# Kernel tuning notes

Measured on AMD Instinct MI355X. Metric: run time of the kernel, lower is better.

## Reference

```python
import jax, jax.numpy as jnp
import numpy as np

N = 100_000      # atoms (nodes)
E = 1_600_000    # directed edges
F_IN = 89        # atom feature dim
H = 128          # hidden dim
P = 20_000       # polyhedra (N/P = 5 atoms each)
C = 500          # crystals (P/C = 40 polyhedra each)
OUT = 1
EPS = 1e-5


def setup_inputs() -> dict:
    key = jax.random.key(0)
    ks = jax.random.split(key, 10)
    x = jax.random.normal(ks[0], (N, F_IN), jnp.float32)
    edge_index = jax.random.randint(ks[1], (2, E), 0, N)
    # sorted segment ids guaranteeing non-empty segments (faithful to PyG Batch layout)
    batch = jnp.repeat(jnp.arange(P), N // P)          # node -> polyhedron
    crystal_ids = jnp.repeat(jnp.arange(C), P // C)    # polyhedron -> crystal
    # GCNConv weights (glorot-ish) and biases; conv0 maps 89->128, convs 1..4 map 128->128
    W0 = jax.random.normal(ks[2], (F_IN, H), jnp.float32) * (1.0 / np.sqrt(F_IN))
    Ws = jax.random.normal(ks[3], (4, H, H), jnp.float32) * (1.0 / np.sqrt(H))
    bs = jnp.zeros((5, H), jnp.float32)
    # 5 BatchNorm layers
    gammas = jnp.ones((5, H), jnp.float32)
    betas = jnp.zeros((5, H), jnp.float32)
    # predictor MLP
    Wp1 = jax.random.normal(ks[4], (H, H), jnp.float32) * (1.0 / np.sqrt(H))
    bp1 = jnp.zeros((H,), jnp.float32)
    Wp2 = jax.random.normal(ks[5], (H, OUT), jnp.float32) * (1.0 / np.sqrt(H))
    bp2 = jnp.zeros((OUT,), jnp.float32)
    return dict(x=x, edge_index=edge_index, batch=batch, crystal_ids=crystal_ids,
                W0=W0, Ws=Ws, bs=bs, gammas=gammas, betas=betas,
                Wp1=Wp1, bp1=bp1, Wp2=Wp2, bp2=bp2)


def _bn(h, g, b):
    # BatchNorm1d, training mode: biased batch statistics over nodes
    mu = jnp.mean(h, axis=0)
    var = jnp.var(h, axis=0)
    return g * (h - mu) * jax.lax.rsqrt(var + EPS) + b


def reference(x, edge_index, batch, crystal_ids, W0, Ws, bs, gammas, betas, Wp1, bp1, Wp2, bp2):
    # --- GCN normalization with self-loops (shared by all 5 convs) ---
    loops = jnp.arange(N)
    src = jnp.concatenate([edge_index[0], loops])   # [E+N]
    dst = jnp.concatenate([edge_index[1], loops])
    deg = jax.ops.segment_sum(jnp.ones_like(src, jnp.float32), dst, num_segments=N)
    dinv = jnp.where(deg > 0, jax.lax.rsqrt(deg), 0.0)
    norm = (dinv[src] * dinv[dst])[:, None]          # [E+N, 1]

    def conv(h, W, b):
        m = h @ W                                    # [N, H]
        agg = jax.ops.segment_sum(m[src] * norm, dst, num_segments=N)
        return agg + b

    h = jax.nn.relu(_bn(conv(x, W0, bs[0]), gammas[0], betas[0]))
    for i in range(4):
        h = jax.nn.relu(_bn(conv(h, Ws[i], bs[i + 1]), gammas[i + 1], betas[i + 1]))

    # global_mean_pool over polyhedra
    cnt_p = jax.ops.segment_sum(jnp.ones((N,), jnp.float32), batch, num_segments=P)
    poly = jax.ops.segment_sum(h, batch, num_segments=P) / cnt_p[:, None]

    # per-crystal mean of polyhedron reps (vectorized form of the Python loop)
    cnt_c = jax.ops.segment_sum(jnp.ones((P,), jnp.float32), crystal_ids, num_segments=C)
    crys = jax.ops.segment_sum(poly, crystal_ids, num_segments=C) / cnt_c[:, None]

    # predictor MLP (Dropout is identity at inference)
    pred = jax.nn.relu(crys @ Wp1 + bp1) @ Wp2 + bp2   # [C, 1]
    return pred
```

## Files before the change

### kernel.cpp

```cpp
#include <hip/hip_runtime.h>

#define N_ATOMS 100000
#define N_EDGES 1600000
#define F_INDIM 89
#define N_CRYS  500
#define EPSBN   1e-5f
#define DRANGE  12500
#define RBLK    250
#define NSB     400
#define CAPSEG  28160
#define GRP     128
#define NGRP    782
#define B1E     2048
#define NBIN    104
#define IMGMAX  12288

typedef unsigned short u16;
typedef unsigned int   u32;
typedef unsigned long long u64;
typedef __attribute__((ext_vector_type(8))) short short8;
typedef __attribute__((ext_vector_type(4))) float f32x4;
typedef __attribute__((ext_vector_type(4))) unsigned int u32x4;

__device__ __forceinline__ float bf2f(u16 u){ union{u32 i; float f;} v; v.i=((u32)u)<<16; return v.f; }
__device__ __forceinline__ float bflo(u32 u){ union{u32 i; float f;} v; v.i=u<<16; return v.f; }
__device__ __forceinline__ float bfhi(u32 u){ union{u32 i; float f;} v; v.i=u&0xffff0000u; return v.f; }
__device__ __forceinline__ u16 f2bf(float f){
  u32 x=__float_as_uint(f);
  return (u16)((x + 0x7fffu + ((x>>16)&1u))>>16);
}
__device__ __forceinline__ u32 pack2(float a, float b){ return (u32)f2bf(a) | ((u32)f2bf(b)<<16); }
__device__ __forceinline__ float ldf(const void* p, int i, int m){
  return m ? ((const float*)p)[i] : bf2f(((const u16*)p)[i]);
}
__device__ __forceinline__ int fpmode(const void* gammas){ return (((const u16*)gammas)[0]==0) ? 1 : 0; }

__global__ __launch_bounds__(256) void k_bucket(const int* __restrict__ ei, u64* __restrict__ bkt,
                                                int* __restrict__ bcnt, int* __restrict__ degi8){
  __shared__ int lcnt[8], loff[8], lbase[8];
  __shared__ u64 lval[256];
  __shared__ int ldst[256];
  int t = threadIdx.x;
  int seg = blockIdx.x & 7;
  int e = blockIdx.x*256 + t;
  if (t < 8) lcnt[t] = 0;
  __syncthreads();
  int d=0, s=0, rr=0, li=0;
  bool valid = (e < N_EDGES);
  if (valid){
    d = ei[N_EDGES+e]; if ((u32)d >= N_ATOMS) d = 0;
    s = ei[e];         if ((u32)s >= N_ATOMS) s = 0;
    rr = d / DRANGE;
    li = atomicAdd(&lcnt[rr], 1);
    atomicAdd(&degi8[seg*N_ATOMS + d], 1);
  }
  __syncthreads();
  if (t == 0){ int run=0; for (int b=0;b<8;b++){ loff[b]=run; run+=lcnt[b]; } }
  __syncthreads();
  if (t < 8 && lcnt[t] > 0)
    lbase[t] = atomicAdd(&bcnt[seg*64 + t], lcnt[t]);
  __syncthreads();
  if (valid){
    int p = loff[rr] + li;
    lval[p] = ((u64)(u32)d << 32) | (u32)s;
    ldst[p] = (seg*8 + rr)*CAPSEG + lbase[rr] + li;
  }
  __syncthreads();
  int tot = loff[7] + lcnt[7];
  if (t < tot) bkt[ldst[t]] = lval[t];
}

__global__ void k_hist(const int* __restrict__ degi8, int* __restrict__ degi,
                       int* __restrict__ hist, int* __restrict__ blockHist){
  __shared__ int lh[256];
  int t = threadIdx.x, b = blockIdx.x;
  lh[t] = 0; __syncthreads();
  if (t < RBLK){
    int n = b*RBLK + t;
    int dg = 0;
    #pragma unroll
    for (int k=0;k<8;k++) dg += degi8[k*N_ATOMS + n];
    degi[n] = dg;
    atomicAdd(&lh[dg>255?255:dg], 1);
  }
  __syncthreads();
  blockHist[b*256 + t] = lh[t];
  if (lh[t]) atomicAdd(&hist[(b/50)*256 + t], lh[t]);
}

__global__ void k_hist_scan(int* __restrict__ hist){
  __shared__ int s[256];
  int R = blockIdx.x, t = threadIdx.x;
  int own = hist[R*256+t]; s[t] = own; __syncthreads();
  for (int k=1;k<256;k<<=1){ int a=(t>=k)?s[t-k]:0; __syncthreads(); s[t]+=a; __syncthreads(); }
  hist[R*256+t] = s[t] - own;
}

__global__ __launch_bounds__(64) void k_blockoff(const int* __restrict__ blockHist, const int* __restrict__ binBase,
                                                 int* __restrict__ blockOff){
  int bid = blockIdx.x;
  int c = bid & 255, R = bid >> 8;
  int t = threadIdx.x;
  int own = (t<50) ? blockHist[(R*50+t)*256 + c] : 0;
  int v = own;
  #pragma unroll
  for (int k=1;k<64;k<<=1){ int u = __shfl_up(v, k, 64); if (t>=k) v += u; }
  if (t<50) blockOff[(R*50+t)*256 + c] = R*DRANGE + binBase[R*256 + c] + (v - own);
}

__global__ void k_rank(const int* __restrict__ degi, const int* __restrict__ blockOff,
                       int* __restrict__ nodeAt, int* __restrict__ rankOf,
                       float* __restrict__ dinv, float* __restrict__ dinvR){
  __shared__ int boff[256];
  __shared__ int cnt[256];
  int b = blockIdx.x, t = threadIdx.x;
  boff[t] = blockOff[b*256 + t];
  cnt[t] = 0;
  __syncthreads();
  if (t >= RBLK) return;
  int n = b*RBLK + t;
  int dg = degi[n];
  int cd = dg>255?255:dg;
  int li = atomicAdd(&cnt[cd], 1);
  int r = boff[cd] + li;
  nodeAt[r] = n; rankOf[n] = r;
  float di = rsqrtf((float)(dg + 1));
  dinv[n] = di; dinvR[r] = di;
}

__global__ __launch_bounds__(256) void k_scan_partial(const int* __restrict__ degi, const int* __restrict__ nodeAt,
                                                      int* __restrict__ bsum){
  int b=blockIdx.x, t=threadIdx.x;
  int s=0;
  #pragma unroll
  for (int j=0;j<4;j++){
    int i=b*1024 + j*256 + t;
    if(i<N_ATOMS){
      int dg = degi[nodeAt[i]];
      s += (dg+3)&~3;
    }
  }
  __shared__ int red[256];
  red[t]=s; __syncthreads();
  for (int k=128;k>0;k>>=1){ if(t<k) red[t]+=red[t+k]; __syncthreads(); }
  if (t==0) bsum[b]=red[0];
}

__global__ void k_scan_bsum(int* __restrict__ bsum, int nb){
  __shared__ int s[128];
  int t=threadIdx.x;
  int own = (t<nb)? bsum[t]:0;
  s[t]=own; __syncthreads();
  for (int k=1;k<128;k<<=1){ int a=(t>=k)?s[t-k]:0; __syncthreads(); s[t]+=a; __syncthreads(); }
  if (t<nb) bsum[t]=s[t]-own;
}

__global__ __launch_bounds__(256) void k_scan_write(const int* __restrict__ degi, const int* __restrict__ nodeAt,
                                                    const int* __restrict__ bsum,
                                                    int* __restrict__ off){
  int b=blockIdx.x, t=threadIdx.x;
  int base=b*1024+t*4;
  int v[4], s=0;
  #pragma unroll
  for (int j=0;j<4;j++){ int i=base+j; v[j]=(i<N_ATOMS)?((degi[nodeAt[i]]+3)&~3):0; s+=v[j]; }
  __shared__ int ts[256];
  ts[t]=s; __syncthreads();
  for (int k=1;k<256;k<<=1){ int a=(t>=k)?ts[t-k]:0; __syncthreads(); ts[t]+=a; __syncthreads(); }
  int run = ts[t]-s + bsum[b];
  #pragma unroll
  for (int j=0;j<4;j++){
    int i=base+j;
    if (i<=N_ATOMS) off[i]=run;
    run+=v[j];
  }
}

__global__ __launch_bounds__(256) void k_group(const u64* __restrict__ bkt, const int* __restrict__ bcnt,
                                               const int* __restrict__ rankOf, const int* __restrict__ off,
                                               int* __restrict__ cnt2, u64* __restrict__ bkt2){
  __shared__ int lcnt[NBIN], loff[NBIN], gb[NBIN];
  __shared__ u64 lval[B1E];
  __shared__ int ldst[B1E];
  const int t = threadIdx.x;
  const int rr = blockIdx.x & 7;
  const int rest = blockIdx.x >> 3;
  const int seg = rest & 7, ch = rest >> 3;
  const int cnt = bcnt[seg*64 + rr];
  const int e0 = ch*B1E;
  int nloc = cnt - e0; if (nloc < 0) nloc = 0; if (nloc > B1E) nloc = B1E;
  const int g0 = (rr*DRANGE) >> 7;
  if (t < NBIN){ lcnt[t] = 0; }
  __syncthreads();
  const u64* src = bkt + (size_t)(seg*8 + rr)*CAPSEG + e0;
  int rk8[8], s8[8], sl8[8];
  #pragma unroll
  for (int j=0;j<8;j++){
    int i = j*256 + t;
    rk8[j] = -1;
    if (i < nloc){
      u64 v = src[i];
      int rk = rankOf[(int)(v>>32)];
      rk8[j] = rk; s8[j] = (int)(u32)v;
      sl8[j] = atomicAdd(&lcnt[(rk>>7) - g0], 1);
    }
  }
  __syncthreads();
  if (t == 0){
    int run = 0;
    for (int b=0;b<NBIN;b++){ loff[b] = run; run += lcnt[b]; }
  }
  __syncthreads();
  if (t < NBIN && lcnt[t] > 0){
    int g = g0 + t;
    gb[t] = off[g*GRP] + atomicAdd(&cnt2[g], lcnt[t]);
  }
  __syncthreads();
  #pragma unroll
  for (int j=0;j<8;j++){
    if (rk8[j] >= 0){
      int rel = (rk8[j]>>7) - g0;
      int p = loff[rel] + sl8[j];
      lval[p] = ((u64)(u32)rk8[j] << 32) | (u32)s8[j];
      ldst[p] = gb[rel] + sl8[j];
    }
  }
  __syncthreads();
  for (int i=t; i<nloc; i+=256)
    bkt2[ldst[i]] = lval[i];
}

__global__ __launch_bounds__(256) void k_csr(const u64* __restrict__ bkt2, const int* __restrict__ cnt2,
                                             const int* __restrict__ off, u32* __restrict__ csrS){
  __shared__ u32 img[IMGMAX];
  __shared__ int lcur[GRP];
  const int g = blockIdx.x, t = threadIdx.x;
  const int r0 = g*GRP;
  const int r1 = (r0+GRP < N_ATOMS) ? r0+GRP : N_ATOMS;
  const int base = off[r0];
  const int size = off[r1] - base;
  const int n = cnt2[g];
  if (size <= IMGMAX){
    for (int i=t; i<size; i+=256) img[i] = (u32)N_ATOMS;
    if (t < r1-r0) lcur[t] = off[r0+t] - base;
    __syncthreads();
    for (int i=t; i<n; i+=256){
      u64 v = bkt2[(size_t)base + i];
      int p = atomicAdd(&lcur[(int)(v>>32) - r0], 1);
      img[p] = (u32)v;
    }
    __syncthreads();
    uint4* c4 = (uint4*)(csrS + base);
    const uint4* i4 = (const uint4*)img;
    for (int i=t; i<(size>>2); i+=256) c4[i] = i4[i];
  } else {
    if (t < r1-r0) lcur[t] = off[r0+t];
    for (int i=t; i<size; i+=256) csrS[base+i] = (u32)N_ATOMS;
    __syncthreads();
    for (int i=t; i<n; i+=256){
      u64 v = bkt2[(size_t)base + i];
      int p = atomicAdd(&lcur[(int)(v>>32) - r0], 1);
      csrS[p] = (u32)v;
    }
  }
}

__global__ void k_packW(const void* __restrict__ W0, const void* __restrict__ Ws,
                        const void* __restrict__ gammas, u16* __restrict__ dst){
  int L    = blockIdx.x >> 3;
  int tid  = (blockIdx.x & 7)*256 + threadIdx.x;
  int K    = (L==0) ? F_INDIM : 128;
  int Kpad = (L==0) ? 96 : 128;
  if (tid >= (Kpad/32)*8*64) return;
  const void* W = (L==0) ? W0 : Ws;
  int woff = (L==0) ? 0 : (L-1)*128*128;
  int fp32m = fpmode(gammas);
  int lane = tid & 63, sc = tid >> 6;
  int c = sc & 7, s = sc >> 3;
  u16 vals[8];
  #pragma unroll
  for (int j=0;j<8;j++){
    int k  = s*32 + (lane>>4)*8 + j;
    int ch = c*16 + (lane&15);
    float v = (k<K) ? ldf(W, woff + k*128 + ch, fp32m) : 0.f;
    vals[j] = f2bf(v);
  }
  u16* out = dst + (size_t)L*16384;
  *(ushort4*)&out[tid*8]   = *(const ushort4*)&vals[0];
  *(ushort4*)&out[tid*8+4] = *(const ushort4*)&vals[4];
}

#define AROW 136
__global__ __launch_bounds__(256) void k_gemm_mfma(const u16* __restrict__ inA, const void* __restrict__ inX,
                                                   int K, int Kpad, const u16* __restrict__ Wpk,
                                                   const float* __restrict__ statsPrev, int useAct,
                                                   const float* __restrict__ dinv,
                                                   u16* __restrict__ mout,
                                                   const void* __restrict__ gammas,
                                                   const void* __restrict__ betas, int goff){
  __shared__ __align__(16) u16 Al[128*AROW];
  __shared__ float cl[256];
  const int t = threadIdx.x, lane = t & 63, w = t >> 6;
  const int tile = blockIdx.x * 128;

  if (useAct){
    if (t < 128){
      int fp32m = fpmode(gammas);
      float mu  = statsPrev[t] * (1.f/N_ATOMS);
      float var = statsPrev[128+t] * (1.f/N_ATOMS) - mu*mu;
      if (var < 0.f) var = 0.f;
      float sc = ldf(gammas, goff+t, fp32m) / sqrtf(var + EPSBN);
      cl[t]     = sc;
      cl[128+t] = ldf(betas, goff+t, fp32m) - sc*mu;
    }
    __syncthreads();
    const uint4* HA4 = (const uint4*)inA;
    for (int idx=t; idx<128*16; idx+=256){
      int node = idx>>4, q = idx&15;
      int gn = tile+node;
      uint4 v = (gn<N_ATOMS) ? HA4[((size_t)(q>>2)*(N_ATOMS+1) + gn)*4 + (q&3)] : make_uint4(0,0,0,0);
      int kk = q*8;
      u16 r[8];
      r[0]=f2bf(fmaxf(fmaf(cl[kk+0], bflo(v.x), cl[128+kk+0]),0.f));
      r[1]=f2bf(fmaxf(fmaf(cl[kk+1], bfhi(v.x), cl[128+kk+1]),0.f));
      r[2]=f2bf(fmaxf(fmaf(cl[kk+2], bflo(v.y), cl[128+kk+2]),0.f));
      r[3]=f2bf(fmaxf(fmaf(cl[kk+3], bfhi(v.y), cl[128+kk+3]),0.f));
      r[4]=f2bf(fmaxf(fmaf(cl[kk+4], bflo(v.z), cl[128+kk+4]),0.f));
      r[5]=f2bf(fmaxf(fmaf(cl[kk+5], bfhi(v.z), cl[128+kk+5]),0.f));
      r[6]=f2bf(fmaxf(fmaf(cl[kk+6], bflo(v.w), cl[128+kk+6]),0.f));
      r[7]=f2bf(fmaxf(fmaf(cl[kk+7], bfhi(v.w), cl[128+kk+7]),0.f));
      *(uint4*)&Al[node*AROW + kk] = *(const uint4*)&r[0];
    }
  } else {
    int fp32m = fpmode(gammas);
    for (int idx=t; idx<128*96; idx+=256){
      int node = idx/96, kk = idx - node*96;
      int gn = tile+node;
      float v = (kk<K && gn<N_ATOMS) ? ldf(inX, gn*K+kk, fp32m) : 0.f;
      Al[node*AROW + kk] = f2bf(v);
    }
  }
  __syncthreads();

  f32x4 acc[2][8];
  #pragma unroll
  for (int rr=0;rr<2;rr++)
    #pragma unroll
    for (int c=0;c<8;c++) acc[rr][c] = (f32x4){0.f,0.f,0.f,0.f};
  const int row = lane & 15, quad = lane >> 4;

  const int nstep = Kpad >> 5;
  for (int s=0; s<nstep; ++s){
    short8 a0 = *(const short8*)&Al[(w*32+row)*AROW    + s*32 + quad*8];
    short8 a1 = *(const short8*)&Al[(w*32+16+row)*AROW + s*32 + quad*8];
    #pragma unroll
    for (int c=0;c<8;c++){
      short8 b = *(const short8*)&Wpk[(size_t)((s*8+c)*64 + lane)*8];
      acc[0][c] = __builtin_amdgcn_mfma_f32_16x16x32_bf16(a0, b, acc[0][c], 0, 0, 0);
      acc[1][c] = __builtin_amdgcn_mfma_f32_16x16x32_bf16(a1, b, acc[1][c], 0, 0, 0);
    }
  }
  __syncthreads();
  float di[2][4];
  #pragma unroll
  for (int rr=0;rr<2;rr++)
    #pragma unroll
    for (int r=0;r<4;r++){
      int gn = tile + w*32 + rr*16 + quad*4 + r;
      di[rr][r] = (gn<N_ATOMS) ? dinv[gn] : 0.f;
    }
  #pragma unroll
  for (int rr=0;rr<2;rr++)
    #pragma unroll
    for (int c=0;c<8;c++)
      #pragma unroll
      for (int r=0;r<4;r++){
        int node = w*32 + rr*16 + quad*4 + r, ch = c*16 + row;
        Al[node*AROW + ch] = f2bf(di[rr][r]*acc[rr][c][r]);
      }
  __syncthreads();
  for (int idx=t; idx<2048; idx+=256){
    int blk = idx>>9, rem = idx&511, node = rem>>2, part = rem&3;
    int gn = tile+node;
    if (gn < N_ATOMS){
      uint4 v = *(const uint4*)&Al[node*AROW + blk*32 + part*8];
      *(uint4*)&mout[((size_t)blk*(N_ATOMS+1) + gn)*32 + part*8] = v;
    }
  }
  if (blockIdx.x == gridDim.x-1 && t < 16){
    int blk = t>>2, part = t&3;
    *(uint4*)&mout[((size_t)blk*(N_ATOMS+1) + N_ATOMS)*32 + part*8] = make_uint4(0,0,0,0);
  }
}

#define ACC8(r) do{ a[0]+=bflo(r.x); a[1]+=bfhi(r.x); a[2]+=bflo(r.y); a[3]+=bfhi(r.y); \
                    a[4]+=bflo(r.z); a[5]+=bfhi(r.z); a[6]+=bflo(r.w); a[7]+=bfhi(r.w);}while(0)
__global__ __launch_bounds__(256) void k_agg(const u16* __restrict__ m_, const u32* __restrict__ csrS,
                                             const int* __restrict__ off, const int* __restrict__ nodeAt,
                                             const float* __restrict__ dinvR,
                                             u16* __restrict__ agg_, float* __restrict__ stats){
  const int t = threadIdx.x, lane = t & 63, w = t >> 6;
  const int par = lane & 3, p = lane >> 2;
  const int cls = blockIdx.x & 7;
  const int slice = cls >> 1, half = cls & 1;
  const int r = half*50000 + (int)(blockIdx.x >> 3)*64 + w*16 + p;
  const int rlim = half*50000 + 50000;

  const uint4* m4   = (const uint4*)m_ + (size_t)slice*(N_ATOMS+1)*4;
  uint4*       agg4 = (uint4*)agg_     + (size_t)slice*(N_ATOMS+1)*4;

  float a[8], q8[8];
  #pragma unroll
  for (int i=0;i<8;i++){ a[i]=0.f; q8[i]=0.f; }

  if (r < rlim){
    int n = nodeAt[r];
    uint4 sv = m4[(size_t)n*4 + par];
    ACC8(sv);
    int e   = off[r];
    int end = off[r+1];
    if ((end - e) & 4){
      u32x4 iv = *(const u32x4*)(csrS+e);
      uint4 g0 = m4[(size_t)iv[0]*4 + par];
      uint4 g1 = m4[(size_t)iv[1]*4 + par];
      uint4 g2 = m4[(size_t)iv[2]*4 + par];
      uint4 g3 = m4[(size_t)iv[3]*4 + par];
      ACC8(g0); ACC8(g1); ACC8(g2); ACC8(g3);
      e += 4;
    }
    if (e < end){
      u32x4 i0 = *(const u32x4*)(csrS+e), i1 = *(const u32x4*)(csrS+e+4);
      uint4 A0 = m4[(size_t)i0[0]*4 + par];
      uint4 A1 = m4[(size_t)i0[1]*4 + par];
      uint4 A2 = m4[(size_t)i0[2]*4 + par];
      uint4 A3 = m4[(size_t)i0[3]*4 + par];
      uint4 A4 = m4[(size_t)i1[0]*4 + par];
      uint4 A5 = m4[(size_t)i1[1]*4 + par];
      uint4 A6 = m4[(size_t)i1[2]*4 + par];
      uint4 A7 = m4[(size_t)i1[3]*4 + par];
      e += 8;
      bool more = (e < end);
      while (true){
        uint4 B0,B1,B2,B3,B4,B5,B6,B7;
        if (more){
          u32x4 j0 = *(const u32x4*)(csrS+e), j1 = *(const u32x4*)(csrS+e+4);
          B0 = m4[(size_t)j0[0]*4 + par];
          B1 = m4[(size_t)j0[1]*4 + par];
          B2 = m4[(size_t)j0[2]*4 + par];
          B3 = m4[(size_t)j0[3]*4 + par];
          B4 = m4[(size_t)j1[0]*4 + par];
          B5 = m4[(size_t)j1[1]*4 + par];
          B6 = m4[(size_t)j1[2]*4 + par];
          B7 = m4[(size_t)j1[3]*4 + par];
          e += 8;
        }
        ACC8(A0); ACC8(A1); ACC8(A2); ACC8(A3);
        ACC8(A4); ACC8(A5); ACC8(A6); ACC8(A7);
        if (!more) break;
        A0=B0; A1=B1; A2=B2; A3=B3; A4=B4; A5=B5; A6=B6; A7=B7;
        more = (e < end);
      }
    }
    float di = dinvR[r];
    #pragma unroll
    for (int i=0;i<8;i++){ a[i]*=di; q8[i]=a[i]*a[i]; }
    u32x4 o;
    o[0] = pack2(a[0],a[1]); o[1] = pack2(a[2],a[3]);
    o[2] = pack2(a[4],a[5]); o[3] = pack2(a[6],a[7]);
    __builtin_nontemporal_store(o, (u32x4*)&agg4[(size_t)n*4 + par]);
  }
  #pragma unroll
  for (int i=0;i<8;i++){
    float s = a[i], q = q8[i];
    s += __shfl_xor(s, 4, 64);  q += __shfl_xor(q, 4, 64);
    s += __shfl_xor(s, 8, 64);  q += __shfl_xor(q, 8, 64);
    s += __shfl_xor(s, 16, 64); q += __shfl_xor(q, 16, 64);
    s += __shfl_xor(s, 32, 64); q += __shfl_xor(q, 32, 64);
    a[i]=s; q8[i]=q;
  }
  __shared__ float sred[4][64];
  if (lane < 4){
    #pragma unroll
    for (int i=0;i<8;i++){ sred[w][par*8+i]=a[i]; sred[w][32+par*8+i]=q8[i]; }
  }
  __syncthreads();
  if (t < 64){
    float v = sred[0][t]+sred[1][t]+sred[2][t]+sred[3][t];
    int ch = slice*32 + (t & 31);
    atomicAdd(&stats[(t<32 ? ch : 128+ch)], v);
  }
}

__global__ __launch_bounds__(128) void k_pool_mlp(const u16* __restrict__ agg, const float* __restrict__ stats4,
                                                  const void* __restrict__ gammas, const void* __restrict__ betas,
                                                  const void* __restrict__ Wp1, const void* __restrict__ bp1,
                                                  const void* __restrict__ Wp2, const void* __restrict__ bp2,
                                                  void* __restrict__ out){
  int c = blockIdx.x, t = threadIdx.x;
  int fp32m = fpmode(gammas);
  float mu  = stats4[t] * (1.f/N_ATOMS);
  float var = stats4[128+t] * (1.f/N_ATOMS) - mu*mu;
  if (var < 0.f) var = 0.f;
  float sc = ldf(gammas, 512+t, fp32m) / sqrtf(var + EPSBN);
  float tb = ldf(betas, 512+t, fp32m) - sc*mu;
  float sum = 0.f;
  const u16* base = agg + ((size_t)(t>>5)*(N_ATOMS+1) + (size_t)c*200)*32 + (t&31);
  for (int i=0;i<200;i++) sum += fmaxf(fmaf(sc, bf2f(base[(size_t)i*32]), tb), 0.f);
  __shared__ float cr[128];
  cr[t] = sum * (1.f/200.f);
  __syncthreads();
  float hj = ldf(bp1, t, fp32m);
  for (int k=0;k<128;k++) hj = fmaf(cr[k], ldf(Wp1, k*128+t, fp32m), hj);
  hj = fmaxf(hj, 0.f);
  __shared__ float red[128];
  red[t] = hj * ldf(Wp2, t, fp32m);
  __syncthreads();
  for (int s=64;s>0;s>>=1){ if (t<s) red[t]+=red[t+s]; __syncthreads(); }
  if (t==0){
    float r = red[0] + ldf(bp2, 0, fp32m);
    if (fp32m) ((float*)out)[c] = r;
    else       ((u16*) out)[c]  = f2bf(r);
  }
}

extern "C" void kernel_launch(void* const* d_in, const int* in_sizes, int n_in,
                              void* d_out, int out_size, void* d_ws, size_t ws_size,
                              hipStream_t stream){
  const void* x      = d_in[0];
  const int*  ei     = (const int*)d_in[1];
  const void* W0     = d_in[4];
  const void* Ws     = d_in[5];
  const void* gammas = d_in[7];
  const void* betas  = d_in[8];
  const void* Wp1    = d_in[9];
  const void* bp1    = d_in[10];
  const void* Wp2    = d_in[11];
  const void* bp2    = d_in[12];
  (void)in_sizes; (void)n_in; (void)out_size; (void)ws_size;

  char* w = (char*)d_ws;
  size_t o = 0;
  auto take = [&](size_t bytes)->char*{ char* p = w+o; o = (o+bytes+255)&~(size_t)255; return p; };
  int*   off    = (int*)  take((size_t)(N_ATOMS+1)*4);
  float* dinv   = (float*)take((size_t)N_ATOMS*4);
  u32*   csrS   = (u32*)  take((size_t)(N_EDGES+4*N_ATOMS)*4);
  u16*   HA     = (u16*)  take((size_t)(N_ATOMS+1)*128*2);
  u16*   HB     = (u16*)  take((size_t)(N_ATOMS+1)*128*2);
  float* stats5 = (float*)take(5*256*4);
  int*   bsum   = (int*)  take(1024*4);
  u16*   Wpk    = (u16*)  take((size_t)5*16384*2);
  int*   nodeAt = (int*)  take((size_t)N_ATOMS*4);
  float* dinvR  = (float*)take((size_t)N_ATOMS*4);
  int* degi8     = (int*)HB;
  int* degi      = (int*)((char*)HB + 3200000);
  int* hist      = (int*)((char*)HB + 3600000);
  int* bcnt      = (int*)((char*)HB + 3608192);
  int* cnt2      = (int*)((char*)HB + 3610240);
  int* rankOf    = (int*)((char*)HB + 3613696);
  int* blockHist = (int*)((char*)HB + 4013696);
  int* blockOff  = (int*)((char*)HB + 4423296);
  u64* bkt       = (u64*)((char*)HB + 4833024);
  u64* bkt2      = (u64*)HA;

  k_packW<<<40, 256, 0, stream>>>(W0, Ws, gammas, Wpk);

  hipMemsetAsync(degi8, 0, 3613440, stream);
  const int echunks = (N_EDGES+255)/256;
  const int ggrid   = ((CAPSEG+B1E-1)/B1E)*8*8;
  k_bucket<<<echunks, 256, 0, stream>>>(ei, bkt, bcnt, degi8);
  k_hist <<<NSB, 256, 0, stream>>>(degi8, degi, hist, blockHist);
  k_hist_scan<<<8, 256, 0, stream>>>(hist);
  k_blockoff<<<8*256, 64, 0, stream>>>(blockHist, hist, blockOff);
  k_rank <<<NSB, 256, 0, stream>>>(degi, blockOff, nodeAt, rankOf, dinv, dinvR);
  const int nb = (N_ATOMS+1023)/1024;
  k_scan_partial<<<nb, 256, 0, stream>>>(degi, nodeAt, bsum);
  k_scan_bsum   <<<1, 128, 0, stream>>>(bsum, nb);
  k_scan_write  <<<nb, 256, 0, stream>>>(degi, nodeAt, bsum, off);
  k_group<<<ggrid, 256, 0, stream>>>(bkt, bcnt, rankOf, off, cnt2, bkt2);
  k_csr  <<<NGRP, 256, 0, stream>>>(bkt2, cnt2, off, csrS);
  hipMemsetAsync(stats5, 0, 5*256*4, stream);

  const int gemm_grid = (N_ATOMS+127)/128;
  const int agg_grid  = ((50000+63)/64)*8;
  for (int L=0; L<5; ++L){
    const int Kpad = (L==0) ? 96 : 128;
    const int K    = (L==0) ? F_INDIM : 128;
    const float* statsPrev = (L==0) ? stats5 : (stats5 + (size_t)(L-1)*256);
    k_gemm_mfma<<<gemm_grid, 256, 0, stream>>>(HA, x, K, Kpad, Wpk + (size_t)L*16384,
                                               statsPrev, (L==0)?0:1, dinv, HB,
                                               gammas, betas, (L-1)*128);
    k_agg <<<agg_grid, 256, 0, stream>>>(HB, csrS, off, nodeAt, dinvR, HA, stats5 + (size_t)L*256);
  }
  k_pool_mlp<<<N_CRYS, 128, 0, stream>>>(HA, stats5 + 4*256, gammas, betas,
                                         Wp1, bp1, Wp2, bp2, d_out);
}
```

Measured before the change: 714.1 us.

## Replace global atomic degree counting with LDS histograms over bucketed edges

Removes the per-edge global atomicAdd into eight replicated degree arrays inside k_bucket. A new k_count3 kernel rereads the bucketed edges and builds per-range degree histograms in shared memory. It writes them as 32 byte-wide partial copies, which k_hist then sums. This drops the 3.6 MB memset and the scattered global atomics, at the cost of an extra kernel and a second pass over the bucket array. Each partial count is truncated to 8 bits, so it assumes a node never gets more than 255 in-edges within one chunk.

```diff
diff --git a/kernel.cpp b/kernel.cpp
--- a/kernel.cpp
+++ b/kernel.cpp
@@ -9,6 +9,7 @@
 #define RBLK    250
 #define NSB     400
 #define CAPSEG  28160
+#define QCH     7040
 #define GRP     128
 #define NGRP    782
 #define B1E     2048
@@ -17,6 +18,7 @@
 
 typedef unsigned short u16;
 typedef unsigned int   u32;
+typedef unsigned char  u8;
 typedef unsigned long long u64;
 typedef __attribute__((ext_vector_type(8))) short short8;
 typedef __attribute__((ext_vector_type(4))) float f32x4;
@@ -36,7 +38,7 @@
 __device__ __forceinline__ int fpmode(const void* gammas){ return (((const u16*)gammas)[0]==0) ? 1 : 0; }
 
 __global__ __launch_bounds__(256) void k_bucket(const int* __restrict__ ei, u64* __restrict__ bkt,
-                                                int* __restrict__ bcnt, int* __restrict__ degi8){
+                                                int* __restrict__ bcnt){
   __shared__ int lcnt[8], loff[8], lbase[8];
   __shared__ u64 lval[256];
   __shared__ int ldst[256];
@@ -52,7 +54,6 @@
     s = ei[e];         if ((u32)s >= N_ATOMS) s = 0;
     rr = d / DRANGE;
     li = atomicAdd(&lcnt[rr], 1);
-    atomicAdd(&degi8[seg*N_ATOMS + d], 1);
   }
   __syncthreads();
   if (t == 0){ int run=0; for (int b=0;b<8;b++){ loff[b]=run; run+=lcnt[b]; } }
@@ -70,7 +71,31 @@
   if (t < tot) bkt[ldst[t]] = lval[t];
 }
 
-__global__ void k_hist(const int* __restrict__ degi8, int* __restrict__ degi,
+__global__ __launch_bounds__(256) void k_count3(const u64* __restrict__ bkt, const int* __restrict__ bcnt,
+                                                u8* __restrict__ hcopy){
+  __shared__ u32 h[DRANGE];
+  const int t = threadIdx.x;
+  const int rr  = blockIdx.x & 7;
+  const int seg = (blockIdx.x >> 3) & 7;
+  const int q   = blockIdx.x >> 6;
+  for (int i=t; i<DRANGE; i+=256) h[i] = 0;
+  __syncthreads();
+  const int cnt = bcnt[seg*64 + rr];
+  int lo = q*QCH, hi = lo + QCH; if (hi > cnt) hi = cnt;
+  const u64* src = bkt + (size_t)(seg*8 + rr)*CAPSEG;
+  for (int i=lo+t; i<hi; i+=256){
+    int d = (int)(src[i] >> 32);
+    atomicAdd(&h[d - rr*DRANGE], 1u);
+  }
+  __syncthreads();
+  u32* dst = (u32*)(hcopy + (size_t)(seg*4+q)*N_ATOMS + rr*DRANGE);
+  for (int j=t; j<DRANGE/4; j+=256){
+    u32 v = (h[4*j]&255u) | ((h[4*j+1]&255u)<<8) | ((h[4*j+2]&255u)<<16) | ((h[4*j+3]&255u)<<24);
+    dst[j] = v;
+  }
+}
+
+__global__ void k_hist(const u8* __restrict__ hcopy, int* __restrict__ degi,
                        int* __restrict__ hist, int* __restrict__ blockHist){
   __shared__ int lh[256];
   int t = threadIdx.x, b = blockIdx.x;
@@ -79,7 +104,7 @@
     int n = b*RBLK + t;
     int dg = 0;
     #pragma unroll
-    for (int k=0;k<8;k++) dg += degi8[k*N_ATOMS + n];
+    for (int k=0;k<32;k++) dg += hcopy[(size_t)k*N_ATOMS + n];
     degi[n] = dg;
     atomicAdd(&lh[dg>255?255:dg], 1);
   }
@@ -550,24 +575,25 @@
   u16*   Wpk    = (u16*)  take((size_t)5*16384*2);
   int*   nodeAt = (int*)  take((size_t)N_ATOMS*4);
   float* dinvR  = (float*)take((size_t)N_ATOMS*4);
-  int* degi8     = (int*)HB;
-  int* degi      = (int*)((char*)HB + 3200000);
-  int* hist      = (int*)((char*)HB + 3600000);
-  int* bcnt      = (int*)((char*)HB + 3608192);
-  int* cnt2      = (int*)((char*)HB + 3610240);
-  int* rankOf    = (int*)((char*)HB + 3613696);
-  int* blockHist = (int*)((char*)HB + 4013696);
-  int* blockOff  = (int*)((char*)HB + 4423296);
-  u64* bkt       = (u64*)((char*)HB + 4833024);
+  int* hist      = (int*)HB;
+  int* bcnt      = (int*)((char*)HB + 8192);
+  int* cnt2      = (int*)((char*)HB + 10240);
+  u8*  hcopy     = (u8*) ((char*)HB + 16384);
+  int* degi      = (int*)((char*)HB + 3216384);
+  int* rankOf    = (int*)((char*)HB + 3616384);
+  int* blockHist = (int*)((char*)HB + 4016384);
+  int* blockOff  = (int*)((char*)HB + 4425984);
+  u64* bkt       = (u64*)((char*)HB + 4835584);
   u64* bkt2      = (u64*)HA;
 
   k_packW<<<40, 256, 0, stream>>>(W0, Ws, gammas, Wpk);
 
-  hipMemsetAsync(degi8, 0, 3613440, stream);
+  hipMemsetAsync(hist, 0, 13440, stream);
   const int echunks = (N_EDGES+255)/256;
   const int ggrid   = ((CAPSEG+B1E-1)/B1E)*8*8;
-  k_bucket<<<echunks, 256, 0, stream>>>(ei, bkt, bcnt, degi8);
-  k_hist <<<NSB, 256, 0, stream>>>(degi8, degi, hist, blockHist);
+  k_bucket<<<echunks, 256, 0, stream>>>(ei, bkt, bcnt);
+  k_count3<<<256, 256, 0, stream>>>(bkt, bcnt, hcopy);
+  k_hist <<<NSB, 256, 0, stream>>>(hcopy, degi, hist, blockHist);
   k_hist_scan<<<8, 256, 0, stream>>>(hist);
   k_blockoff<<<8*256, 64, 0, stream>>>(blockHist, hist, blockOff);
   k_rank <<<NSB, 256, 0, stream>>>(degi, blockOff, nodeAt, rankOf, dinv, dinvR);
```

After: 670.0 us. 1.07x faster.
